# Kernel tuning notes

Hardware: AMD Instinct MI355X
Metric: run time of the kernel (lower is better)

The kernel has to match this reference:

```python
import jax, jax.numpy as jnp
import numpy as np

B, S, H, I, E, TOP_K, CAP = 4, 2048, 1024, 256, 256, 2, 256


def setup_inputs() -> dict:
    key = jax.random.key(0)
    ks = jax.random.split(key, 5)
    return {
        "hidden_states": jax.random.normal(ks[0], (B, S, H), dtype=jnp.float32),
        "router_w": jax.random.normal(ks[1], (E, H), dtype=jnp.float32) * 0.02,
        "w_gate": jax.random.normal(ks[2], (E, H, I), dtype=jnp.float32) * 0.02,
        "w_up": jax.random.normal(ks[3], (E, H, I), dtype=jnp.float32) * 0.02,
        "w_down": jax.random.normal(ks[4], (E, I, H), dtype=jnp.float32) * 0.02,
        "gate_scale": jnp.ones((E,), dtype=jnp.float32),
        "up_scale": jnp.ones((E,), dtype=jnp.float32),
        "down_scale": jnp.ones((E,), dtype=jnp.float32),
    }


def reference(hidden_states, router_w, w_gate, w_up, w_down, gate_scale, up_scale, down_scale):
    # ---- Router: softmax over experts, top-k, renormalize selected scores ----
    logits = jnp.einsum("bsh,eh->bse", hidden_states, router_w)
    probs = jax.nn.softmax(logits, axis=-1)
    scores, indices = jax.lax.top_k(probs, TOP_K)          # [B,S,K]
    scores = jax.nn.softmax(scores, axis=-1)

    T = B * S
    N = T * TOP_K
    x_flat = hidden_states.reshape(T, H)
    e_ids = indices.reshape(N)                              # expert per assignment
    wts = scores.reshape(N)

    # ---- Dispatch: position of each assignment within its expert's group ----
    onehot = (e_ids[:, None] == jnp.arange(E)[None, :]).astype(jnp.int32)  # [N,E]
    pos = jnp.take_along_axis(jnp.cumsum(onehot, axis=0), e_ids[:, None], axis=1)[:, 0] - 1
    pos = jnp.minimum(pos, CAP - 1)  # CAP=256 >> mean load 64; overflow never hit in practice

    x_a = jnp.repeat(x_flat, TOP_K, axis=0)                 # [N,H] assignment inputs
    x_buf = jnp.zeros((E, CAP, H), dtype=hidden_states.dtype).at[e_ids, pos].set(x_a)

    # ---- Per-expert SwiGLU MLP (grouped GEMMs), with scale_inv buffers ----
    gate = jnp.einsum("ech,ehi->eci", x_buf, w_gate) * gate_scale[:, None, None]
    up = jnp.einsum("ech,ehi->eci", x_buf, w_up) * up_scale[:, None, None]
    y_buf = jnp.einsum("eci,eih->ech", jax.nn.silu(gate) * up, w_down) * down_scale[:, None, None]

    # ---- Combine: gather back, weight by routing score, sum over top-k ----
    y = y_buf[e_ids, pos] * wts[:, None]                    # [N,H]
    out = y.reshape(T, TOP_K, H).sum(axis=1).reshape(B, S, H)
    return out
```

## Files before the change

### kernel.cpp

```cpp
#include <hip/hip_runtime.h>
#include <hip/hip_bf16.h>


#define T_TOK 8192
#define H_DIM 1024
#define I_DIM 256
#define E_NUM 256
#define CAPc  256

typedef short short8 __attribute__((ext_vector_type(8)));
typedef float f32x4  __attribute__((ext_vector_type(4)));

__device__ __forceinline__ short f2b(float f) {
    unsigned int u = __float_as_uint(f);
    u += 0x7FFFu + ((u >> 16) & 1u);
    return (short)(u >> 16);
}
__device__ __forceinline__ unsigned int pack2(float a, float b) {
    return (unsigned int)(unsigned short)f2b(a) | ((unsigned int)(unsigned short)f2b(b) << 16);
}

__global__ void zero_cnt_kernel(int4* __restrict__ cnt4) {
    cnt4[threadIdx.x] = make_int4(0, 0, 0, 0);
}
__global__ void zero_out_kernel(float4* __restrict__ out4, int n4) {
    int idx = blockIdx.x * blockDim.x + threadIdx.x;
    float4 z = make_float4(0.f, 0.f, 0.f, 0.f);
    int stride = gridDim.x * blockDim.x;
    for (int i = idx; i < n4; i += stride) out4[i] = z;
}

__global__ __launch_bounds__(256) void router_gemm(const float* __restrict__ x,
                                                   const float* __restrict__ rw,
                                                   float* __restrict__ logits) {
    __shared__ float xb[64 * 36];
    __shared__ float wb[64 * 36];
    const int tid = threadIdx.x;
    const int m0 = (int)(blockIdx.x >> 2) * 64;
    const int e0 = (int)(blockIdx.x & 3) * 64;
    const int tx = tid & 15, ty = tid >> 4;
    float acc[4][4];
#pragma unroll
    for (int i = 0; i < 4; ++i)
#pragma unroll
        for (int j = 0; j < 4; ++j) acc[i][j] = 0.f;

    const int r0 = tid >> 3, s4 = (tid & 7) * 4;
    for (int k0 = 0; k0 < H_DIM; k0 += 32) {
        __syncthreads();
#pragma unroll
        for (int p = 0; p < 2; ++p) {
            int r = p * 32 + r0;
            *(float4*)&xb[r * 36 + s4] = *(const float4*)&x[(size_t)(m0 + r) * H_DIM + k0 + s4];
            *(float4*)&wb[r * 36 + s4] = *(const float4*)&rw[(size_t)(e0 + r) * H_DIM + k0 + s4];
        }
        __syncthreads();
#pragma unroll 2
        for (int kk = 0; kk < 32; kk += 4) {
            float4 xr[4], wr[4];
#pragma unroll
            for (int i = 0; i < 4; ++i) xr[i] = *(const float4*)&xb[(ty + 16 * i) * 36 + kk];
#pragma unroll
            for (int j = 0; j < 4; ++j) wr[j] = *(const float4*)&wb[(tx + 16 * j) * 36 + kk];
#pragma unroll
            for (int i = 0; i < 4; ++i)
#pragma unroll
                for (int j = 0; j < 4; ++j)
                    acc[i][j] += xr[i].x * wr[j].x + xr[i].y * wr[j].y +
                                 xr[i].z * wr[j].z + xr[i].w * wr[j].w;
        }
    }
#pragma unroll
    for (int i = 0; i < 4; ++i)
#pragma unroll
        for (int j = 0; j < 4; ++j)
            logits[(size_t)(m0 + ty + 16 * i) * E_NUM + (e0 + tx + 16 * j)] = acc[i][j];
}

__global__ __launch_bounds__(256) void topk_kernel(const float* __restrict__ logits,
                                                   int* __restrict__ cnt,
                                                   int* __restrict__ tok_of,
                                                   float* __restrict__ wt_of) {
    const int t = blockIdx.x * 4 + (threadIdx.x >> 6);
    const int l = threadIdx.x & 63;
    float4 lv = *(const float4*)&logits[(size_t)t * E_NUM + l * 4];
    float mx = fmaxf(fmaxf(lv.x, lv.y), fmaxf(lv.z, lv.w));
    for (int o = 32; o; o >>= 1) mx = fmaxf(mx, __shfl_xor(mx, o));
    float se = __expf(lv.x - mx) + __expf(lv.y - mx) + __expf(lv.z - mx) + __expf(lv.w - mx);
    for (int o = 32; o; o >>= 1) se += __shfl_xor(se, o);
    float vals[4] = {lv.x, lv.y, lv.z, lv.w};
    float v1 = -3.4e38f, v2 = -3.4e38f;
    int i1 = 0x7fffffff, i2 = 0x7fffffff;
#pragma unroll
    for (int c = 0; c < 4; ++c) {
        float v = vals[c]; int idx = l * 4 + c;
        if (v > v1 || (v == v1 && idx < i1)) { v2 = v1; i2 = i1; v1 = v; i1 = idx; }
        else if (v > v2 || (v == v2 && idx < i2)) { v2 = v; i2 = idx; }
    }
    for (int o = 1; o < 64; o <<= 1) {
        float ov1 = __shfl_xor(v1, o); int oi1 = __shfl_xor(i1, o);
        float ov2 = __shfl_xor(v2, o); int oi2 = __shfl_xor(i2, o);
        if (ov1 > v1 || (ov1 == v1 && oi1 < i1)) {
            float nv2; int ni2;
            if (v1 > ov2 || (v1 == ov2 && i1 < oi2)) { nv2 = v1; ni2 = i1; }
            else { nv2 = ov2; ni2 = oi2; }
            v1 = ov1; i1 = oi1; v2 = nv2; i2 = ni2;
        } else {
            if (ov1 > v2 || (ov1 == v2 && oi1 < i2)) { v2 = ov1; i2 = oi1; }
        }
    }
    if (l == 0) {
        float p1 = __expf(v1 - mx) / se;
        float p2 = __expf(v2 - mx) / se;
        float ew = __expf(p2 - p1);
        float w1 = 1.f / (1.f + ew);
        float w2 = ew / (1.f + ew);
        int s1 = atomicAdd(&cnt[i1], 1); if (s1 > CAPc - 1) s1 = CAPc - 1;
        tok_of[i1 * CAPc + s1] = 2 * t;     wt_of[i1 * CAPc + s1] = w1;
        int s2 = atomicAdd(&cnt[i2], 1); if (s2 > CAPc - 1) s2 = CAPc - 1;
        tok_of[i2 * CAPc + s2] = 2 * t + 1; wt_of[i2 * CAPc + s2] = w2;
    }
}

__global__ __launch_bounds__(512, 2) void expert_kernel(
    const float* __restrict__ x, const float* __restrict__ wg, const float* __restrict__ wu,
    const float* __restrict__ wd, const float* __restrict__ gsc, const float* __restrict__ usc,
    const float* __restrict__ dsc, const int* __restrict__ cnt, const int* __restrict__ tok_of,
    const float* __restrict__ wt_of, float* __restrict__ out, float* __restrict__ y_ws,
    const int use_ws) {
    __shared__ __attribute__((aligned(16))) char lds[102400];
    short* xs   = (short*)(lds);
    short* wgs  = (short*)(lds + 10240);
    short* wus  = (short*)(lds + 27648);
    short* acts = (short*)(lds);
    short* wds  = (short*)(lds + 67584);
    int*   toks = (int*)(lds + 101376);
    float* wts  = (float*)(lds + 101888);

    const int e = blockIdx.x;
    int c = cnt[e]; if (c > CAPc) c = CAPc;
    if (c == 0) return;
    const float gse = gsc[e], use_ = usc[e], dse = dsc[e];
    const int tid = threadIdx.x;
    const int w = tid >> 6, l = tid & 63, l15 = l & 15, lq = l >> 4;
    const size_t wbase = (size_t)e * (H_DIM * I_DIM);
    const f32x4 z4 = {0.f, 0.f, 0.f, 0.f};

    for (int mc = 0; mc * 128 < c; ++mc) {
        const int rows = min(128, c - mc * 128);
        __syncthreads();
        if (tid < rows) {
            toks[tid] = tok_of[e * CAPc + mc * 128 + tid];
            wts[tid]  = wt_of[e * CAPc + mc * 128 + tid];
        }
        __syncthreads();

        f32x4 accg[8][2], accu[8][2];
#pragma unroll
        for (int i = 0; i < 8; ++i)
#pragma unroll
            for (int j = 0; j < 2; ++j) { accg[i][j] = z4; accu[i][j] = z4; }

        const int xr0 = tid >> 3, xc4 = (tid & 7) * 4;
        const int r1 = xr0, r2 = 64 + xr0;
        const size_t xb1 = (r1 < rows) ? (size_t)(toks[r1] >> 1) * H_DIM : 0;
        const size_t xb2 = (r2 < rows) ? (size_t)(toks[r2] >> 1) * H_DIM : 0;
        const bool v1 = (r1 < rows), v2 = (r2 < rows);

        for (int ko = 0; ko < 32; ++ko) {
            __syncthreads();
            {
                unsigned int lo = 0, hi = 0;
                if (v1) { float4 v = *(const float4*)&x[xb1 + ko * 32 + xc4];
                          lo = pack2(v.x, v.y); hi = pack2(v.z, v.w); }
                *(uint2*)&xs[r1 * 40 + xc4] = make_uint2(lo, hi);
                lo = 0; hi = 0;
                if (v2) { float4 v = *(const float4*)&x[xb2 + ko * 32 + xc4];
                          lo = pack2(v.x, v.y); hi = pack2(v.z, v.w); }
                *(uint2*)&xs[r2 * 40 + xc4] = make_uint2(lo, hi);
            }
#pragma unroll
            for (int s = 0; s < 4; ++s) {
                int f4 = s * 512 + tid;
                int k = f4 >> 6, c4 = (f4 & 63) * 4;
                size_t ga = wbase + (size_t)(ko * 32 + k) * I_DIM + c4;
                float4 vg = *(const float4*)&wg[ga];
                float4 vu = *(const float4*)&wu[ga];
                *(uint2*)&wgs[k * 272 + c4] = make_uint2(pack2(vg.x, vg.y), pack2(vg.z, vg.w));
                *(uint2*)&wus[k * 272 + c4] = make_uint2(pack2(vu.x, vu.y), pack2(vu.z, vu.w));
            }
            __syncthreads();
            short8 a[8];
#pragma unroll
            for (int mt = 0; mt < 8; ++mt)
                a[mt] = *(const short8*)&xs[(mt * 16 + l15) * 40 + lq * 8];
#pragma unroll
            for (int nt = 0; nt < 2; ++nt) {
                const int col = w * 32 + nt * 16 + l15;
                short8 bg, bu;
#pragma unroll
                for (int j = 0; j < 8; ++j) {
                    bg[j] = wgs[(lq * 8 + j) * 272 + col];
                    bu[j] = wus[(lq * 8 + j) * 272 + col];
                }
#pragma unroll
                for (int mt = 0; mt < 8; ++mt) {
                    accg[mt][nt] = __builtin_amdgcn_mfma_f32_16x16x32_bf16(a[mt], bg, accg[mt][nt], 0, 0, 0);
                    accu[mt][nt] = __builtin_amdgcn_mfma_f32_16x16x32_bf16(a[mt], bu, accu[mt][nt], 0, 0, 0);
                }
            }
        }

        __syncthreads();
#pragma unroll
        for (int mt = 0; mt < 8; ++mt)
#pragma unroll
            for (int nt = 0; nt < 2; ++nt) {
                const int col = w * 32 + nt * 16 + l15;
#pragma unroll
                for (int r = 0; r < 4; ++r) {
                    const int row = mt * 16 + lq * 4 + r;
                    float g = accg[mt][nt][r] * gse;
                    float u = accu[mt][nt][r] * use_;
                    acts[row * 264 + col] = f2b((g / (1.f + __expf(-g))) * u);
                }
            }

        for (int half = 0; half < 2; ++half) {
            f32x4 acc[8][4];
#pragma unroll
            for (int i = 0; i < 8; ++i)
#pragma unroll
                for (int j = 0; j < 4; ++j) acc[i][j] = z4;
            for (int ki = 0; ki < 8; ++ki) {
                __syncthreads();
#pragma unroll
                for (int s = 0; s < 8; ++s) {
                    int f4 = s * 512 + tid;
                    int k = f4 >> 7, c4 = (f4 & 127) * 4;
                    float4 v = *(const float4*)&wd[(size_t)e * (I_DIM * H_DIM) +
                                                   (size_t)(ki * 32 + k) * H_DIM + half * 512 + c4];
                    *(uint2*)&wds[k * 528 + c4] = make_uint2(pack2(v.x, v.y), pack2(v.z, v.w));
                }
                __syncthreads();
                short8 a[8];
#pragma unroll
                for (int mt = 0; mt < 8; ++mt)
                    a[mt] = *(const short8*)&acts[(mt * 16 + l15) * 264 + ki * 32 + lq * 8];
#pragma unroll
                for (int nt = 0; nt < 4; ++nt) {
                    const int coll = w * 64 + nt * 16 + l15;
                    short8 b;
#pragma unroll
                    for (int j = 0; j < 8; ++j) b[j] = wds[(lq * 8 + j) * 528 + coll];
#pragma unroll
                    for (int mt = 0; mt < 8; ++mt)
                        acc[mt][nt] = __builtin_amdgcn_mfma_f32_16x16x32_bf16(a[mt], b, acc[mt][nt], 0, 0, 0);
                }
            }
#pragma unroll
            for (int mt = 0; mt < 8; ++mt)
#pragma unroll
                for (int r = 0; r < 4; ++r) {
                    const int row = mt * 16 + lq * 4 + r;
                    if (row < rows) {
                        const float wrow = dse * wts[row];
                        const int tk = toks[row];
#pragma unroll
                        for (int nt = 0; nt < 4; ++nt) {
                            const int col = half * 512 + w * 64 + nt * 16 + l15;
                            float v = acc[mt][nt][r] * wrow;
                            if (use_ws) y_ws[(size_t)tk * H_DIM + col] = v;
                            else atomicAdd(&out[(size_t)(tk >> 1) * H_DIM + col], v);
                        }
                    }
                }
        }
    }
}

__global__ __launch_bounds__(256) void combine_kernel(const float4* __restrict__ y4,
                                                      float4* __restrict__ out4) {
    const int t = blockIdx.x;
    const int i = threadIdx.x;
    float4 a = y4[(size_t)t * 512 + i];
    float4 b = y4[(size_t)t * 512 + 256 + i];
    out4[(size_t)t * 256 + i] = make_float4(a.x + b.x, a.y + b.y, a.z + b.z, a.w + b.w);
}

extern "C" void kernel_launch(void* const* d_in, const int* in_sizes, int n_in,
                              void* d_out, int out_size, void* d_ws, size_t ws_size,
                              hipStream_t stream) {
    const float* x  = (const float*)d_in[0];
    const float* rw = (const float*)d_in[1];
    const float* wg = (const float*)d_in[2];
    const float* wu = (const float*)d_in[3];
    const float* wd = (const float*)d_in[4];
    const float* gs = (const float*)d_in[5];
    const float* us = (const float*)d_in[6];
    const float* ds = (const float*)d_in[7];
    float* out = (float*)d_out;

    char* ws = (char*)d_ws;
    float* logits = (float*)ws;
    int*   cnt    = (int*)(ws + 8388608);
    int*   tok_of = (int*)(ws + 8389632);
    float* wt_of  = (float*)(ws + 8651776);
    float* y_ws   = (float*)(ws + 8913920);
    const size_t need = 8913920ull + 67108864ull;
    const int use_ws = (ws_size >= need) ? 1 : 0;

    zero_cnt_kernel<<<1, 64, 0, stream>>>((int4*)cnt);
    if (!use_ws)
        zero_out_kernel<<<2048, 256, 0, stream>>>((float4*)out, (T_TOK * H_DIM) / 4);
    router_gemm<<<512, 256, 0, stream>>>(x, rw, logits);
    topk_kernel<<<2048, 256, 0, stream>>>(logits, cnt, tok_of, wt_of);
    expert_kernel<<<E_NUM, 512, 0, stream>>>(x, wg, wu, wd, gs, us, ds, cnt, tok_of, wt_of,
                                             out, y_ws, use_ws);
    if (use_ws)
        combine_kernel<<<T_TOK, 256, 0, stream>>>((const float4*)y_ws, (float4*)out);
}
```

Measured before the change: 1.007 ms.

## Double-buffer expert GEMM tiles in LDS and double the block to 1024 threads

The expert kernel now runs 1024 threads per block, so each wave owns a narrower column slice. Both the gate/up GEMM and the down GEMM stage their tiles through two LDS buffers: the next tile's global loads are issued before the current tile's MFMAs, and the packed bf16 data is written to the other buffer afterwards, leaving one barrier per k-step. This is meant to hide global load latency behind matrix math. In exchange LDS use grows to about 133 KB per block and there are fewer accumulators per wave, and launch_bounds(1024,4) may not be achievable and could cost registers.

```diff
diff --git a/kernel.cpp b/kernel.cpp
--- a/kernel.cpp
+++ b/kernel.cpp
@@ -122,20 +122,101 @@
     }
 }
 
-__global__ __launch_bounds__(512, 2) void expert_kernel(
+#define XS_OFF(p)  ((p) * 43520)
+#define WG_OFF(p)  ((p) * 43520 + 10240)
+#define WU_OFF(p)  ((p) * 43520 + 26880)
+#define ACT_OFF    0
+#define WDS_OFF(p) (67584 + (p) * 33536)
+#define TOK_OFF    134656
+#define WTS_OFF    135168
+#define LDS_TOTAL  135680
+
+#define P1_LOAD(ko_) do {                                                           \
+    xr_ = xval ? *(const float4*)&x[xb + (ko_) * 32 + xc4]                          \
+               : make_float4(0.f, 0.f, 0.f, 0.f);                                   \
+    _Pragma("unroll")                                                               \
+    for (int s = 0; s < 2; ++s) {                                                   \
+        const int f4 = s * 1024 + tid, k = f4 >> 6, c4_ = (f4 & 63) * 4;            \
+        const size_t ga = wbase + (size_t)((ko_) * 32 + k) * I_DIM + c4_;           \
+        gv[s] = *(const float4*)&wg[ga];                                            \
+        uv[s] = *(const float4*)&wu[ga];                                            \
+    } } while (0)
+
+#define P1_WRITE(p_) do {                                                           \
+    short* xs_ = (short*)(lds + XS_OFF(p_));                                        \
+    short* gs_ = (short*)(lds + WG_OFF(p_));                                        \
+    short* us_ = (short*)(lds + WU_OFF(p_));                                        \
+    *(uint2*)&xs_[xrow * 40 + xc4] =                                                \
+        make_uint2(pack2(xr_.x, xr_.y), pack2(xr_.z, xr_.w));                       \
+    _Pragma("unroll")                                                               \
+    for (int s = 0; s < 2; ++s) {                                                   \
+        const int f4 = s * 1024 + tid, k = f4 >> 6, c4_ = (f4 & 63) * 4;            \
+        *(uint2*)&gs_[k * 260 + c4_] =                                              \
+            make_uint2(pack2(gv[s].x, gv[s].y), pack2(gv[s].z, gv[s].w));           \
+        *(uint2*)&us_[k * 260 + c4_] =                                              \
+            make_uint2(pack2(uv[s].x, uv[s].y), pack2(uv[s].z, uv[s].w));           \
+    } } while (0)
+
+#define P1_COMP(p_) do {                                                            \
+    const short* xs_ = (const short*)(lds + XS_OFF(p_));                            \
+    const short* gs_ = (const short*)(lds + WG_OFF(p_));                            \
+    const short* us_ = (const short*)(lds + WU_OFF(p_));                            \
+    const int col_ = w * 16 + l15;                                                  \
+    short8 bg, bu;                                                                  \
+    _Pragma("unroll")                                                               \
+    for (int j = 0; j < 8; ++j) {                                                   \
+        bg[j] = gs_[(lq * 8 + j) * 260 + col_];                                     \
+        bu[j] = us_[(lq * 8 + j) * 260 + col_];                                     \
+    }                                                                               \
+    _Pragma("unroll")                                                               \
+    for (int mt = 0; mt < 8; ++mt) {                                                \
+        short8 a_ = *(const short8*)&xs_[(mt * 16 + l15) * 40 + lq * 8];            \
+        accg[mt] = __builtin_amdgcn_mfma_f32_16x16x32_bf16(a_, bg, accg[mt], 0, 0, 0); \
+        accu[mt] = __builtin_amdgcn_mfma_f32_16x16x32_bf16(a_, bu, accu[mt], 0, 0, 0); \
+    } } while (0)
+
+#define P2_LOAD(half_, ki_) do {                                                    \
+    _Pragma("unroll")                                                               \
+    for (int s = 0; s < 4; ++s) {                                                   \
+        const int f4 = s * 1024 + tid, k = f4 >> 7, c4_ = (f4 & 127) * 4;           \
+        dv[s] = *(const float4*)&wd[dbase + (size_t)((ki_) * 32 + k) * H_DIM +      \
+                                    (half_) * 512 + c4_];                           \
+    } } while (0)
+
+#define P2_WRITE(p_) do {                                                           \
+    short* ws_ = (short*)(lds + WDS_OFF(p_));                                       \
+    _Pragma("unroll")                                                               \
+    for (int s = 0; s < 4; ++s) {                                                   \
+        const int f4 = s * 1024 + tid, k = f4 >> 7, c4_ = (f4 & 127) * 4;           \
+        *(uint2*)&ws_[k * 524 + c4_] =                                              \
+            make_uint2(pack2(dv[s].x, dv[s].y), pack2(dv[s].z, dv[s].w));           \
+    } } while (0)
+
+#define P2_COMP(p_, ki_) do {                                                       \
+    const short* ws_ = (const short*)(lds + WDS_OFF(p_));                           \
+    const short* ac_ = (const short*)(lds + ACT_OFF);                               \
+    short8 b0, b1;                                                                  \
+    _Pragma("unroll")                                                               \
+    for (int j = 0; j < 8; ++j) {                                                   \
+        b0[j] = ws_[(lq * 8 + j) * 524 + (w * 32 + l15)];                           \
+        b1[j] = ws_[(lq * 8 + j) * 524 + (w * 32 + 16 + l15)];                      \
+    }                                                                               \
+    _Pragma("unroll")                                                               \
+    for (int mt = 0; mt < 8; ++mt) {                                                \
+        short8 a_ = *(const short8*)&ac_[(mt * 16 + l15) * 264 + (ki_) * 32 + lq * 8]; \
+        acc[mt][0] = __builtin_amdgcn_mfma_f32_16x16x32_bf16(a_, b0, acc[mt][0], 0, 0, 0); \
+        acc[mt][1] = __builtin_amdgcn_mfma_f32_16x16x32_bf16(a_, b1, acc[mt][1], 0, 0, 0); \
+    } } while (0)
+
+__global__ __launch_bounds__(1024, 4) void expert_kernel(
     const float* __restrict__ x, const float* __restrict__ wg, const float* __restrict__ wu,
     const float* __restrict__ wd, const float* __restrict__ gsc, const float* __restrict__ usc,
     const float* __restrict__ dsc, const int* __restrict__ cnt, const int* __restrict__ tok_of,
     const float* __restrict__ wt_of, float* __restrict__ out, float* __restrict__ y_ws,
     const int use_ws) {
-    __shared__ __attribute__((aligned(16))) char lds[102400];
-    short* xs   = (short*)(lds);
-    short* wgs  = (short*)(lds + 10240);
-    short* wus  = (short*)(lds + 27648);
-    short* acts = (short*)(lds);
-    short* wds  = (short*)(lds + 67584);
-    int*   toks = (int*)(lds + 101376);
-    float* wts  = (float*)(lds + 101888);
+    __shared__ __attribute__((aligned(16))) char lds[LDS_TOTAL];
+    int*   toks = (int*)(lds + TOK_OFF);
+    float* wts  = (float*)(lds + WTS_OFF);
 
     const int e = blockIdx.x;
     int c = cnt[e]; if (c > CAPc) c = CAPc;
@@ -144,119 +225,68 @@
     const int tid = threadIdx.x;
     const int w = tid >> 6, l = tid & 63, l15 = l & 15, lq = l >> 4;
     const size_t wbase = (size_t)e * (H_DIM * I_DIM);
+    const size_t dbase = (size_t)e * (I_DIM * H_DIM);
     const f32x4 z4 = {0.f, 0.f, 0.f, 0.f};
 
     for (int mc = 0; mc * 128 < c; ++mc) {
         const int rows = min(128, c - mc * 128);
         __syncthreads();
-        if (tid < rows) {
-            toks[tid] = tok_of[e * CAPc + mc * 128 + tid];
-            wts[tid]  = wt_of[e * CAPc + mc * 128 + tid];
-        }
-        __syncthreads();
-
-        f32x4 accg[8][2], accu[8][2];
-#pragma unroll
-        for (int i = 0; i < 8; ++i)
-#pragma unroll
-            for (int j = 0; j < 2; ++j) { accg[i][j] = z4; accu[i][j] = z4; }
-
-        const int xr0 = tid >> 3, xc4 = (tid & 7) * 4;
-        const int r1 = xr0, r2 = 64 + xr0;
-        const size_t xb1 = (r1 < rows) ? (size_t)(toks[r1] >> 1) * H_DIM : 0;
-        const size_t xb2 = (r2 < rows) ? (size_t)(toks[r2] >> 1) * H_DIM : 0;
-        const bool v1 = (r1 < rows), v2 = (r2 < rows);
-
+        if (tid < 128) {
+            const int idx = mc * 128 + tid;
+            toks[tid] = (idx < c) ? tok_of[e * CAPc + idx] : 0;
+            wts[tid]  = (idx < c) ? wt_of[e * CAPc + idx] : 0.f;
+        }
+        __syncthreads();
+
+        const int xrow = tid >> 3, xc4 = (tid & 7) * 4;
+        const bool xval = (xrow < rows);
+        const size_t xb = xval ? (size_t)(toks[xrow] >> 1) * H_DIM : 0;
+
+        f32x4 accg[8], accu[8];
+#pragma unroll
+        for (int i = 0; i < 8; ++i) { accg[i] = z4; accu[i] = z4; }
+        float4 xr_, gv[2], uv[2];
+
+        P1_LOAD(0);
+        P1_WRITE(0);
+        __syncthreads();
         for (int ko = 0; ko < 32; ++ko) {
+            const int p = ko & 1;
+            if (ko < 31) P1_LOAD(ko + 1);
+            P1_COMP(p);
+            if (ko < 31) P1_WRITE(p ^ 1);
             __syncthreads();
-            {
-                unsigned int lo = 0, hi = 0;
-                if (v1) { float4 v = *(const float4*)&x[xb1 + ko * 32 + xc4];
-                          lo = pack2(v.x, v.y); hi = pack2(v.z, v.w); }
-                *(uint2*)&xs[r1 * 40 + xc4] = make_uint2(lo, hi);
-                lo = 0; hi = 0;
-                if (v2) { float4 v = *(const float4*)&x[xb2 + ko * 32 + xc4];
-                          lo = pack2(v.x, v.y); hi = pack2(v.z, v.w); }
-                *(uint2*)&xs[r2 * 40 + xc4] = make_uint2(lo, hi);
-            }
-#pragma unroll
-            for (int s = 0; s < 4; ++s) {
-                int f4 = s * 512 + tid;
-                int k = f4 >> 6, c4 = (f4 & 63) * 4;
-                size_t ga = wbase + (size_t)(ko * 32 + k) * I_DIM + c4;
-                float4 vg = *(const float4*)&wg[ga];
-                float4 vu = *(const float4*)&wu[ga];
-                *(uint2*)&wgs[k * 272 + c4] = make_uint2(pack2(vg.x, vg.y), pack2(vg.z, vg.w));
-                *(uint2*)&wus[k * 272 + c4] = make_uint2(pack2(vu.x, vu.y), pack2(vu.z, vu.w));
-            }
-            __syncthreads();
-            short8 a[8];
+        }
+
+        {
+            short* acts = (short*)(lds + ACT_OFF);
+            const int colA = w * 16 + l15;
 #pragma unroll
             for (int mt = 0; mt < 8; ++mt)
-                a[mt] = *(const short8*)&xs[(mt * 16 + l15) * 40 + lq * 8];
-#pragma unroll
-            for (int nt = 0; nt < 2; ++nt) {
-                const int col = w * 32 + nt * 16 + l15;
-                short8 bg, bu;
-#pragma unroll
-                for (int j = 0; j < 8; ++j) {
-                    bg[j] = wgs[(lq * 8 + j) * 272 + col];
-                    bu[j] = wus[(lq * 8 + j) * 272 + col];
-                }
-#pragma unroll
-                for (int mt = 0; mt < 8; ++mt) {
-                    accg[mt][nt] = __builtin_amdgcn_mfma_f32_16x16x32_bf16(a[mt], bg, accg[mt][nt], 0, 0, 0);
-                    accu[mt][nt] = __builtin_amdgcn_mfma_f32_16x16x32_bf16(a[mt], bu, accu[mt][nt], 0, 0, 0);
-                }
-            }
-        }
-
-        __syncthreads();
-#pragma unroll
-        for (int mt = 0; mt < 8; ++mt)
-#pragma unroll
-            for (int nt = 0; nt < 2; ++nt) {
-                const int col = w * 32 + nt * 16 + l15;
 #pragma unroll
                 for (int r = 0; r < 4; ++r) {
                     const int row = mt * 16 + lq * 4 + r;
-                    float g = accg[mt][nt][r] * gse;
-                    float u = accu[mt][nt][r] * use_;
-                    acts[row * 264 + col] = f2b((g / (1.f + __expf(-g))) * u);
+                    float g = accg[mt][r] * gse;
+                    float u = accu[mt][r] * use_;
+                    acts[row * 264 + colA] = f2b((g / (1.f + __expf(-g))) * u);
                 }
-            }
+        }
+        __syncthreads();
 
         for (int half = 0; half < 2; ++half) {
-            f32x4 acc[8][4];
-#pragma unroll
-            for (int i = 0; i < 8; ++i)
-#pragma unroll
-                for (int j = 0; j < 4; ++j) acc[i][j] = z4;
+            f32x4 acc[8][2];
+#pragma unroll
+            for (int i = 0; i < 8; ++i) { acc[i][0] = z4; acc[i][1] = z4; }
+            float4 dv[4];
+            P2_LOAD(half, 0);
+            P2_WRITE(0);
+            __syncthreads();
             for (int ki = 0; ki < 8; ++ki) {
+                const int p = ki & 1;
+                if (ki < 7) P2_LOAD(half, ki + 1);
+                P2_COMP(p, ki);
+                if (ki < 7) P2_WRITE(p ^ 1);
                 __syncthreads();
-#pragma unroll
-                for (int s = 0; s < 8; ++s) {
-                    int f4 = s * 512 + tid;
-                    int k = f4 >> 7, c4 = (f4 & 127) * 4;
-                    float4 v = *(const float4*)&wd[(size_t)e * (I_DIM * H_DIM) +
-                                                   (size_t)(ki * 32 + k) * H_DIM + half * 512 + c4];
-                    *(uint2*)&wds[k * 528 + c4] = make_uint2(pack2(v.x, v.y), pack2(v.z, v.w));
-                }
-                __syncthreads();
-                short8 a[8];
-#pragma unroll
-                for (int mt = 0; mt < 8; ++mt)
-                    a[mt] = *(const short8*)&acts[(mt * 16 + l15) * 264 + ki * 32 + lq * 8];
-#pragma unroll
-                for (int nt = 0; nt < 4; ++nt) {
-                    const int coll = w * 64 + nt * 16 + l15;
-                    short8 b;
-#pragma unroll
-                    for (int j = 0; j < 8; ++j) b[j] = wds[(lq * 8 + j) * 528 + coll];
-#pragma unroll
-                    for (int mt = 0; mt < 8; ++mt)
-                        acc[mt][nt] = __builtin_amdgcn_mfma_f32_16x16x32_bf16(a[mt], b, acc[mt][nt], 0, 0, 0);
-                }
             }
 #pragma unroll
             for (int mt = 0; mt < 8; ++mt)
@@ -267,8 +297,8 @@
                         const float wrow = dse * wts[row];
                         const int tk = toks[row];
 #pragma unroll
-                        for (int nt = 0; nt < 4; ++nt) {
-                            const int col = half * 512 + w * 64 + nt * 16 + l15;
+                        for (int nt = 0; nt < 2; ++nt) {
+                            const int col = half * 512 + w * 32 + nt * 16 + l15;
                             float v = acc[mt][nt][r] * wrow;
                             if (use_ws) y_ws[(size_t)tk * H_DIM + col] = v;
                             else atomicAdd(&out[(size_t)(tk >> 1) * H_DIM + col], v);
@@ -315,8 +345,8 @@
         zero_out_kernel<<<2048, 256, 0, stream>>>((float4*)out, (T_TOK * H_DIM) / 4);
     router_gemm<<<512, 256, 0, stream>>>(x, rw, logits);
     topk_kernel<<<2048, 256, 0, stream>>>(logits, cnt, tok_of, wt_of);
-    expert_kernel<<<E_NUM, 512, 0, stream>>>(x, wg, wu, wd, gs, us, ds, cnt, tok_of, wt_of,
-                                             out, y_ws, use_ws);
+    expert_kernel<<<E_NUM, 1024, 0, stream>>>(x, wg, wu, wd, gs, us, ds, cnt, tok_of, wt_of,
+                                              out, y_ws, use_ws);
     if (use_ws)
         combine_kernel<<<T_TOK, 256, 0, stream>>>((const float4*)y_ws, (float4*)out);
 }
```

After: 1.020 ms. Within noise of the previous version (+1.3%).
